# Performance work log

Measured on AMD Instinct MI355X. Metric: run time of the kernel, lower is better.

The kernel has to match this reference:

```python
import jax, jax.numpy as jnp
import numpy as np

HIDDEN = 1024
INTER = 2048
NUM_EXPERTS = 8
TOP_K = 2
GROUP_SIZE = 128
TOKENS = 4096


def _dequant_int4(packed, scale, group_size):
    # packed: [E, N, K//2] ints in [0,256) holding two uint4 nibbles (low | high<<4)
    # scale:  [E, N, K//group_size] float32
    E, N, Kh = packed.shape
    K = 2 * Kh
    low = packed & 0xF
    high = (packed >> 4) & 0xF
    # interleave: even K positions = low nibble, odd = high nibble
    q = jnp.stack([low, high], axis=-1).reshape(E, N, K) - 8  # int4 values in [-8,7]
    q = q.astype(jnp.float32).reshape(E, N, K // group_size, group_size)
    w = q * scale[..., None]
    return w.reshape(E, N, K)


def setup_inputs() -> dict:
    key = jax.random.key(0)
    k1, k2, k3, k4, k5, k6 = jax.random.split(key, 6)
    x = jax.random.normal(k1, (TOKENS, HIDDEN), dtype=jnp.float32)
    router_w = jax.random.normal(k2, (NUM_EXPERTS, HIDDEN), dtype=jnp.float32) * 0.02
    w1 = jax.random.randint(k3, (NUM_EXPERTS, 2 * INTER, HIDDEN // 2), 0, 256, dtype=jnp.int32)
    w1_scale = jax.random.uniform(k4, (NUM_EXPERTS, 2 * INTER, HIDDEN // GROUP_SIZE), dtype=jnp.float32) * 0.05
    w2 = jax.random.randint(k5, (NUM_EXPERTS, HIDDEN, INTER // 2), 0, 256, dtype=jnp.int32)
    w2_scale = jax.random.uniform(k6, (NUM_EXPERTS, HIDDEN, INTER // GROUP_SIZE), dtype=jnp.float32) * 0.05
    return {"x": x, "router_w": router_w, "w1": w1, "w1_scale": w1_scale, "w2": w2, "w2_scale": w2_scale}


def reference(x, router_w, w1, w1_scale, w2, w2_scale):
    # Router: topk then softmax over the top-k logits
    scores = x @ router_w.T                                 # [T, E]
    top_w, top_i = jax.lax.top_k(scores, TOP_K)             # [T, K]
    top_w = jax.nn.softmax(top_w, axis=-1).astype(jnp.float32)

    # Dequantize int4 grouped weights once
    w1_deq = _dequant_int4(w1, w1_scale, GROUP_SIZE)        # [E, 2I, H]
    w2_deq = _dequant_int4(w2, w2_scale, GROUP_SIZE)        # [E, H, I]

    out = jnp.zeros_like(x)
    for e in range(NUM_EXPERTS):
        # per-token routing weight for expert e (0 if not routed)
        ge = jnp.sum(top_w * (top_i == e), axis=-1)         # [T]
        h = x @ w1_deq[e].T                                  # [T, 2I]
        gate, up = h[:, :INTER], h[:, INTER:]
        a = jax.nn.silu(gate) * up                           # SwiGLU
        y = a @ w2_deq[e].T                                  # [T, H]
        out = out + ge[:, None] * y
    return out
```

## Files before the change

### kernel.cpp

```cpp
#include <hip/hip_runtime.h>
#include <hip/hip_bf16.h>

#define HIDDEN 1024
#define INTER 2048
#define NE 8
#define GS 128
#define TOKENS 4096
#define MAXROWS 9216
#define MAXTILES 72
#define MAXT256 40

typedef __bf16 bf16x8 __attribute__((ext_vector_type(8)));
typedef float f32x4 __attribute__((ext_vector_type(4)));

#define OFF_TOPKI 0u
#define OFF_TOPKW 32768u
#define OFF_CTRL  65536u
#define OFF_TOK   66048u
#define OFF_SLOT  102912u
#define OFF_TILE  135680u
#define OFF_T256  136192u
#define OFF_V256  136448u
#define OFF_XB    139776u
#define OFF_A     8530432u
#define OFF_W1D   46279168u
#define OFF_W2D   113388032u
#define OFF_Y0    OFF_W1D
#define OFF_Y1    (OFF_W1D + 18874368u)

__device__ __forceinline__ unsigned short f2bf(float f) {
  union { float f; unsigned int u; } v; v.f = f;
  unsigned int r = (v.u + 0x7FFFu + ((v.u >> 16) & 1u)) >> 16;
  return (unsigned short)r;
}
__device__ __forceinline__ float bf2f(unsigned int u) {
  union { unsigned int u; float f; } v; v.u = u << 16;
  return v.f;
}
__device__ __forceinline__ unsigned int pack2(unsigned short lo, unsigned short hi) {
  return (unsigned int)lo | ((unsigned int)hi << 16);
}

typedef const __attribute__((address_space(1))) unsigned int GAS;
typedef __attribute__((address_space(3))) unsigned int LAS;
__device__ __forceinline__ void gload16(const unsigned short* g, unsigned short* l) {
  __builtin_amdgcn_global_load_lds((GAS*)g, (LAS*)l, 16, 0, 0);
}

__global__ __launch_bounds__(256) void k_prep(const float* __restrict__ x,
    const float* __restrict__ rw, int* __restrict__ topki, float* __restrict__ topkw,
    const int* __restrict__ w1, const float* __restrict__ w1s,
    unsigned short* __restrict__ w1d,
    const int* __restrict__ w2, const float* __restrict__ w2s,
    unsigned short* __restrict__ w2d, unsigned short* __restrict__ xb) {
  int bid = blockIdx.x, tid = threadIdx.x;
  if (bid == 7168) {
    uint2 z; z.x = 0u; z.y = 0u;
    *reinterpret_cast<uint2*>(xb + (size_t)TOKENS * HIDDEN + tid * 4) = z;
    return;
  }
  if (bid >= 5120) {
    size_t base = (size_t)(bid - 5120) * 4096 + tid * 4;
    int4 p[4];
#pragma unroll
    for (int c = 0; c < 4; c++)
      p[c] = *reinterpret_cast<const int4*>(w2 + base + c * 1024);
#pragma unroll
    for (int c = 0; c < 4; c++) {
      size_t i4 = base + c * 1024;
      int r = (int)(i4 >> 10);
      int i = (int)(i4 & 1023);
      float s = w2s[r * 16 + (i >> 6)];
      int pv[4] = { p[c].x, p[c].y, p[c].z, p[c].w };
      uint4 o; unsigned int ov[4];
#pragma unroll
      for (int j = 0; j < 4; j++) {
        float lo = (float)((pv[j] & 15) - 8) * s;
        float hi = (float)(((pv[j] >> 4) & 15) - 8) * s;
        ov[j] = pack2(f2bf(lo), f2bf(hi));
      }
      o.x = ov[0]; o.y = ov[1]; o.z = ov[2]; o.w = ov[3];
      *reinterpret_cast<uint4*>(w2d + 2 * i4) = o;
    }
    return;
  }
  if (bid >= 1024) {
    size_t base = (size_t)(bid - 1024) * 4096 + tid * 4;
    int4 p[4];
#pragma unroll
    for (int c = 0; c < 4; c++)
      p[c] = *reinterpret_cast<const int4*>(w1 + base + c * 1024);
#pragma unroll
    for (int c = 0; c < 4; c++) {
      size_t i4 = base + c * 1024;
      int r = (int)(i4 >> 9);
      int i = (int)(i4 & 511);
      float s = w1s[r * 8 + (i >> 6)];
      int pv[4] = { p[c].x, p[c].y, p[c].z, p[c].w };
      uint4 o; unsigned int ov[4];
#pragma unroll
      for (int j = 0; j < 4; j++) {
        float lo = (float)((pv[j] & 15) - 8) * s;
        float hi = (float)(((pv[j] >> 4) & 15) - 8) * s;
        ov[j] = pack2(f2bf(lo), f2bf(hi));
      }
      o.x = ov[0]; o.y = ov[1]; o.z = ov[2]; o.w = ov[3];
      *reinterpret_cast<uint4*>(w1d + 2 * i4) = o;
    }
    return;
  }
  int wave = tid >> 6, lane = tid & 63;
  int t = bid * 4 + wave;
  const float* xr = x + (size_t)t * HIDDEN;
  float acc[NE];
#pragma unroll
  for (int e = 0; e < NE; e++) acc[e] = 0.f;
#pragma unroll
  for (int j = 0; j < 4; j++) {
    int col = j * 256 + lane * 4;
    float4 xv = *reinterpret_cast<const float4*>(xr + col);
    uint2 o;
    o.x = pack2(f2bf(xv.x), f2bf(xv.y));
    o.y = pack2(f2bf(xv.z), f2bf(xv.w));
    *reinterpret_cast<uint2*>(xb + (size_t)t * HIDDEN + col) = o;
#pragma unroll
    for (int e = 0; e < NE; e++) {
      float4 wv = *reinterpret_cast<const float4*>(rw + e * HIDDEN + col);
      acc[e] += xv.x * wv.x + xv.y * wv.y + xv.z * wv.z + xv.w * wv.w;
    }
  }
#pragma unroll
  for (int e = 0; e < NE; e++) {
    float v = acc[e];
    for (int off = 32; off > 0; off >>= 1) v += __shfl_down(v, off, 64);
    acc[e] = v;
  }
  if (lane == 0) {
    int b0 = 0; float s0 = acc[0];
#pragma unroll
    for (int e = 1; e < NE; e++) if (acc[e] > s0) { s0 = acc[e]; b0 = e; }
    int b1 = -1; float s1 = -3.0e38f;
#pragma unroll
    for (int e = 0; e < NE; e++) if (e != b0 && acc[e] > s1) { s1 = acc[e]; b1 = e; }
    float w0 = 1.f / (1.f + __expf(s1 - s0));
    topki[t * 2] = b0; topki[t * 2 + 1] = b1;
    topkw[t * 2] = w0; topkw[t * 2 + 1] = 1.f - w0;
  }
}

__global__ __launch_bounds__(256) void k_route2(const int* __restrict__ topki,
    int* __restrict__ ctrl, int* __restrict__ tok, int* __restrict__ slots,
    int* __restrict__ tilemap, int* __restrict__ tile256, int* __restrict__ valid256) {
  __shared__ int h[NE], off[NE], cnt[NE];
  int tid = threadIdx.x;
  if (tid < NE) h[tid] = 0;
  __syncthreads();
  for (int i = tid; i < TOKENS * 2; i += 256) atomicAdd(&h[topki[i]], 1);
  __syncthreads();
  if (tid == 0) {
    int run = 0, t = 0, t2 = 0;
    for (int e = 0; e < NE; e++) {
      int c = h[e];
      ctrl[e] = c; ctrl[16 + e] = run; off[e] = run;
      int pc = (c + 127) & ~127;
      int m = pc >> 7;
      for (int mt = 0; mt < m; mt++) tilemap[t++] = (e << 20) | (run + mt * 128);
      int n2 = (m + 1) >> 1;
      for (int i2 = 0; i2 < n2; i2++) {
        int st = i2 * 256;
        if (st + 256 > pc) st = (pc >= 256) ? (pc - 256) : 0;
        tile256[t2] = (e << 20) | (run + st);
        int v = pc - st; valid256[t2] = (v < 256) ? v : 256;
        t2++;
      }
      run += pc;
    }
    ctrl[24] = run; ctrl[25] = t; ctrl[26] = t2;
  }
  __syncthreads();
#pragma unroll
  for (int e = 0; e < NE; e++) {
    int c = h[e], pc = (c + 127) & ~127;
    for (int i = c + tid; i < pc; i += 256) tok[off[e] + i] = -1;
  }
  if (tid < NE) cnt[tid] = off[tid];
  __syncthreads();
  for (int i = tid; i < TOKENS * 2; i += 256) {
    int e = topki[i];
    int p = atomicAdd(&cnt[e], 1);
    tok[p] = i >> 1;
    slots[i] = p;
  }
}

__global__ __launch_bounds__(256) void k_gemm1(
    const unsigned short* __restrict__ xb, const unsigned short* __restrict__ w1d,
    const int* __restrict__ ctrl, const int* __restrict__ tilemap,
    const int* __restrict__ tok, unsigned short* __restrict__ a_out) {
  __shared__ unsigned short sA[128 * 32];
  __shared__ unsigned short sBg[64 * 32];
  __shared__ unsigned short sBu[64 * 32];
  int bid = blockIdx.x, tid = threadIdx.x;
  int nt = bid & 31, tile = bid >> 5;
  if (tile >= ctrl[25]) return;
  int tm = tilemap[tile];
  int e = tm >> 20, row0 = tm & 0xFFFFF;
  int n0 = nt * 64;
  int wave = tid >> 6, lane = tid & 63;
  int ln = lane & 15, quad = lane >> 4;
  int wr = (wave & 1) * 64, wc = (wave >> 1) * 32;

  int srow = tid >> 2, scblk = tid & 3;
  int scol = (scblk ^ ((srow >> 1) & 3)) * 8;
  int t0 = tok[row0 + srow];
  int t1 = tok[row0 + 64 + srow];
  const unsigned short* gA0 = xb + (size_t)(t0 < 0 ? TOKENS : t0) * HIDDEN + scol;
  const unsigned short* gA1 = xb + (size_t)(t1 < 0 ? TOKENS : t1) * HIDDEN + scol;
  const unsigned short* gBg = w1d + ((size_t)e * 4096 + n0 + srow) * HIDDEN + scol;
  const unsigned short* gBu = gBg + (size_t)INTER * HIDDEN;
  unsigned short* lA0 = sA + tid * 8;
  unsigned short* lA1 = sA + 64 * 32 + tid * 8;
  unsigned short* lBg = sBg + tid * 8;
  unsigned short* lBu = sBu + tid * 8;

  f32x4 aG[4][2] = {}, aU[4][2] = {};
  for (int k0 = 0; k0 < HIDDEN; k0 += 32) {
    __syncthreads();
    gload16(gA0 + k0, lA0);
    gload16(gA1 + k0, lA1);
    gload16(gBg + k0, lBg);
    gload16(gBu + k0, lBu);
    __syncthreads();
    bf16x8 af[4], bg[2], bu[2];
#pragma unroll
    for (int m = 0; m < 4; m++) {
      int ar = wr + m * 16 + ln;
      af[m] = *reinterpret_cast<const bf16x8*>(&sA[ar * 32 + (quad ^ ((ar >> 1) & 3)) * 8]);
    }
#pragma unroll
    for (int n = 0; n < 2; n++) {
      int br = wc + n * 16 + ln;
      int bo = br * 32 + (quad ^ ((br >> 1) & 3)) * 8;
      bg[n] = *reinterpret_cast<const bf16x8*>(&sBg[bo]);
      bu[n] = *reinterpret_cast<const bf16x8*>(&sBu[bo]);
    }
#pragma unroll
    for (int m = 0; m < 4; m++)
#pragma unroll
      for (int n = 0; n < 2; n++) {
        aG[m][n] = __builtin_amdgcn_mfma_f32_16x16x32_bf16(af[m], bg[n], aG[m][n], 0, 0, 0);
        aU[m][n] = __builtin_amdgcn_mfma_f32_16x16x32_bf16(af[m], bu[n], aU[m][n], 0, 0, 0);
      }
  }
#pragma unroll
  for (int m = 0; m < 4; m++)
#pragma unroll
    for (int n = 0; n < 2; n++) {
      int col = n0 + wc + n * 16 + ln;
#pragma unroll
      for (int r = 0; r < 4; r++) {
        float g = aG[m][n][r], u = aU[m][n][r];
        float act = (g / (1.f + __expf(-g))) * u;
        int row = row0 + wr + m * 16 + quad * 4 + r;
        a_out[(size_t)row * INTER + col] = f2bf(act);
      }
    }
}

__global__ __launch_bounds__(256) void k_gemm2(
    const unsigned short* __restrict__ a_in, const unsigned short* __restrict__ w2d,
    const int* __restrict__ ctrl, const int* __restrict__ tilemap,
    unsigned short* __restrict__ y) {
  __shared__ unsigned short sA[128 * 32];
  __shared__ unsigned short sB[128 * 32];
  int bid = blockIdx.x, tid = threadIdx.x;
  int kp = bid & 1, nt = (bid >> 1) & 7, tile = bid >> 4;
  if (tile >= ctrl[25]) return;
  int tm = tilemap[tile];
  int e = tm >> 20, row0 = tm & 0xFFFFF;
  int n0 = nt * 128;
  int wave = tid >> 6, lane = tid & 63;
  int ln = lane & 15, quad = lane >> 4;
  int wr = (wave & 1) * 64, wc = (wave >> 1) * 64;

  int srow = tid >> 2, scblk = tid & 3;
  int scol = (scblk ^ ((srow >> 1) & 3)) * 8;
  int kbase = kp * (INTER / 2);
  const unsigned short* gA0 = a_in + (size_t)(row0 + srow) * INTER + kbase + scol;
  const unsigned short* gA1 = gA0 + (size_t)64 * INTER;
  const unsigned short* gB0 = w2d + ((size_t)e * 1024 + n0 + srow) * INTER + kbase + scol;
  const unsigned short* gB1 = gB0 + (size_t)64 * INTER;
  unsigned short* lA0 = sA + tid * 8;
  unsigned short* lA1 = sA + 64 * 32 + tid * 8;
  unsigned short* lB0 = sB + tid * 8;
  unsigned short* lB1 = sB + 64 * 32 + tid * 8;

  f32x4 acc[4][4] = {};
  for (int k0 = 0; k0 < INTER / 2; k0 += 32) {
    __syncthreads();
    gload16(gA0 + k0, lA0);
    gload16(gA1 + k0, lA1);
    gload16(gB0 + k0, lB0);
    gload16(gB1 + k0, lB1);
    __syncthreads();
    bf16x8 af[4], bf_[4];
#pragma unroll
    for (int m = 0; m < 4; m++) {
      int ar = wr + m * 16 + ln;
      af[m] = *reinterpret_cast<const bf16x8*>(&sA[ar * 32 + (quad ^ ((ar >> 1) & 3)) * 8]);
    }
#pragma unroll
    for (int n = 0; n < 4; n++) {
      int br = wc + n * 16 + ln;
      bf_[n] = *reinterpret_cast<const bf16x8*>(&sB[br * 32 + (quad ^ ((br >> 1) & 3)) * 8]);
    }
#pragma unroll
    for (int m = 0; m < 4; m++)
#pragma unroll
      for (int n = 0; n < 4; n++)
        acc[m][n] = __builtin_amdgcn_mfma_f32_16x16x32_bf16(af[m], bf_[n], acc[m][n], 0, 0, 0);
  }
  unsigned short* yk = y + (size_t)kp * MAXROWS * HIDDEN;
#pragma unroll
  for (int m = 0; m < 4; m++)
#pragma unroll
    for (int n = 0; n < 4; n++) {
      int col = n0 + wc + n * 16 + ln;
#pragma unroll
      for (int r = 0; r < 4; r++) {
        int row = row0 + wr + m * 16 + quad * 4 + r;
        yk[(size_t)row * HIDDEN + col] = f2bf(acc[m][n][r]);
      }
    }
}

__global__ __launch_bounds__(256) void k_combine(const unsigned short* __restrict__ y,
    const int* __restrict__ slots, const float* __restrict__ topkw,
    float* __restrict__ out) {
  int t = blockIdx.x;
  int c = threadIdx.x * 4;
  int s0 = slots[t * 2], s1 = slots[t * 2 + 1];
  float g0 = topkw[t * 2], g1 = topkw[t * 2 + 1];
  const unsigned short* y1 = y + (size_t)MAXROWS * HIDDEN;
  uint2 a0 = *reinterpret_cast<const uint2*>(y  + (size_t)s0 * HIDDEN + c);
  uint2 a1 = *reinterpret_cast<const uint2*>(y1 + (size_t)s0 * HIDDEN + c);
  uint2 b0 = *reinterpret_cast<const uint2*>(y  + (size_t)s1 * HIDDEN + c);
  uint2 b1 = *reinterpret_cast<const uint2*>(y1 + (size_t)s1 * HIDDEN + c);
  float4 o;
  o.x = g0 * (bf2f(a0.x & 0xffffu) + bf2f(a1.x & 0xffffu))
      + g1 * (bf2f(b0.x & 0xffffu) + bf2f(b1.x & 0xffffu));
  o.y = g0 * (bf2f(a0.x >> 16) + bf2f(a1.x >> 16))
      + g1 * (bf2f(b0.x >> 16) + bf2f(b1.x >> 16));
  o.z = g0 * (bf2f(a0.y & 0xffffu) + bf2f(a1.y & 0xffffu))
      + g1 * (bf2f(b0.y & 0xffffu) + bf2f(b1.y & 0xffffu));
  o.w = g0 * (bf2f(a0.y >> 16) + bf2f(a1.y >> 16))
      + g1 * (bf2f(b0.y >> 16) + bf2f(b1.y >> 16));
  *reinterpret_cast<float4*>(out + (size_t)t * HIDDEN + c) = o;
}

extern "C" void kernel_launch(void* const* d_in, const int* in_sizes, int n_in,
                              void* d_out, int out_size, void* d_ws, size_t ws_size,
                              hipStream_t stream) {
  const float* x   = (const float*)d_in[0];
  const float* rw  = (const float*)d_in[1];
  const int*   w1  = (const int*)d_in[2];
  const float* w1s = (const float*)d_in[3];
  const int*   w2  = (const int*)d_in[4];
  const float* w2s = (const float*)d_in[5];
  float* out = (float*)d_out;
  char* ws = (char*)d_ws;

  int*   topki = (int*)(ws + OFF_TOPKI);
  float* topkw = (float*)(ws + OFF_TOPKW);
  int*   ctrl  = (int*)(ws + OFF_CTRL);
  int*   tok   = (int*)(ws + OFF_TOK);
  int*   slots = (int*)(ws + OFF_SLOT);
  int*   tilemap = (int*)(ws + OFF_TILE);
  int*   tile256 = (int*)(ws + OFF_T256);
  int*   valid256 = (int*)(ws + OFF_V256);
  unsigned short* xb  = (unsigned short*)(ws + OFF_XB);
  unsigned short* a   = (unsigned short*)(ws + OFF_A);
  unsigned short* w1d = (unsigned short*)(ws + OFF_W1D);
  unsigned short* w2d = (unsigned short*)(ws + OFF_W2D);
  unsigned short* y   = (unsigned short*)(ws + OFF_Y0);

  k_prep<<<7169, 256, 0, stream>>>(x, rw, topki, topkw, w1, w1s, w1d, w2, w2s, w2d, xb);
  k_route2<<<1, 256, 0, stream>>>(topki, ctrl, tok, slots, tilemap, tile256, valid256);
  k_gemm1<<<32 * MAXTILES, 256, 0, stream>>>(xb, w1d, ctrl, tilemap, tok, a);
  k_gemm2<<<16 * MAXTILES, 256, 0, stream>>>(a, w2d, ctrl, tilemap, y);
  k_combine<<<TOKENS, 256, 0, stream>>>(y, slots, topkw, out);
}
```

Before: 325.7 us.

## Fuse int4 weight dequantization into both expert GEMM B-tile loads

Drops the separate pass that expanded all int4 weights to bf16 in a workspace buffer. Each GEMM block now loads packed int32 words and dequantizes them in registers with a magic-number float trick and a packed bf16 convert, then writes the bf16 values to shared memory. This removes a large write and re-read of bf16 weights in exchange for repeated dequant work in every block that shares an expert's weights. The B loads also become synchronous register loads instead of direct-to-LDS loads, which may stall more per k-step.

```diff
diff --git a/kernel.cpp b/kernel.cpp
--- a/kernel.cpp
+++ b/kernel.cpp
@@ -23,10 +23,8 @@
 #define OFF_V256  136448u
 #define OFF_XB    139776u
 #define OFF_A     8530432u
-#define OFF_W1D   46279168u
-#define OFF_W2D   113388032u
-#define OFF_Y0    OFF_W1D
-#define OFF_Y1    (OFF_W1D + 18874368u)
+#define OFF_Y0    46279168u
+#define OFF_Y1    (OFF_Y0 + 18874368u)
 
 __device__ __forceinline__ unsigned short f2bf(float f) {
   union { float f; unsigned int u; } v; v.f = f;
@@ -47,66 +45,32 @@
   __builtin_amdgcn_global_load_lds((GAS*)g, (LAS*)l, 16, 0, 0);
 }
 
+__device__ __forceinline__ uint4 deq8(int4 p, float s, float c) {
+  unsigned int pv[4] = { (unsigned int)p.x, (unsigned int)p.y,
+                         (unsigned int)p.z, (unsigned int)p.w };
+  unsigned int ov[4];
+#pragma unroll
+  for (int j = 0; j < 4; j++) {
+    unsigned int v = pv[j];
+    float flo = __uint_as_float(0x43000000u | ((v & 15u) << 16));
+    float fhi = __uint_as_float(0x43000000u | ((v << 12) & 0x000F0000u));
+    float lo = __builtin_fmaf(flo, s, c);
+    float hi = __builtin_fmaf(fhi, s, c);
+    unsigned int pk;
+    asm("v_cvt_pk_bf16_f32 %0, %1, %2" : "=v"(pk) : "v"(lo), "v"(hi));
+    ov[j] = pk;
+  }
+  uint4 o; o.x = ov[0]; o.y = ov[1]; o.z = ov[2]; o.w = ov[3];
+  return o;
+}
+
 __global__ __launch_bounds__(256) void k_prep(const float* __restrict__ x,
     const float* __restrict__ rw, int* __restrict__ topki, float* __restrict__ topkw,
-    const int* __restrict__ w1, const float* __restrict__ w1s,
-    unsigned short* __restrict__ w1d,
-    const int* __restrict__ w2, const float* __restrict__ w2s,
-    unsigned short* __restrict__ w2d, unsigned short* __restrict__ xb) {
+    unsigned short* __restrict__ xb) {
   int bid = blockIdx.x, tid = threadIdx.x;
-  if (bid == 7168) {
+  if (bid == 1024) {
     uint2 z; z.x = 0u; z.y = 0u;
     *reinterpret_cast<uint2*>(xb + (size_t)TOKENS * HIDDEN + tid * 4) = z;
-    return;
-  }
-  if (bid >= 5120) {
-    size_t base = (size_t)(bid - 5120) * 4096 + tid * 4;
-    int4 p[4];
-#pragma unroll
-    for (int c = 0; c < 4; c++)
-      p[c] = *reinterpret_cast<const int4*>(w2 + base + c * 1024);
-#pragma unroll
-    for (int c = 0; c < 4; c++) {
-      size_t i4 = base + c * 1024;
-      int r = (int)(i4 >> 10);
-      int i = (int)(i4 & 1023);
-      float s = w2s[r * 16 + (i >> 6)];
-      int pv[4] = { p[c].x, p[c].y, p[c].z, p[c].w };
-      uint4 o; unsigned int ov[4];
-#pragma unroll
-      for (int j = 0; j < 4; j++) {
-        float lo = (float)((pv[j] & 15) - 8) * s;
-        float hi = (float)(((pv[j] >> 4) & 15) - 8) * s;
-        ov[j] = pack2(f2bf(lo), f2bf(hi));
-      }
-      o.x = ov[0]; o.y = ov[1]; o.z = ov[2]; o.w = ov[3];
-      *reinterpret_cast<uint4*>(w2d + 2 * i4) = o;
-    }
-    return;
-  }
-  if (bid >= 1024) {
-    size_t base = (size_t)(bid - 1024) * 4096 + tid * 4;
-    int4 p[4];
-#pragma unroll
-    for (int c = 0; c < 4; c++)
-      p[c] = *reinterpret_cast<const int4*>(w1 + base + c * 1024);
-#pragma unroll
-    for (int c = 0; c < 4; c++) {
-      size_t i4 = base + c * 1024;
-      int r = (int)(i4 >> 9);
-      int i = (int)(i4 & 511);
-      float s = w1s[r * 8 + (i >> 6)];
-      int pv[4] = { p[c].x, p[c].y, p[c].z, p[c].w };
-      uint4 o; unsigned int ov[4];
-#pragma unroll
-      for (int j = 0; j < 4; j++) {
-        float lo = (float)((pv[j] & 15) - 8) * s;
-        float hi = (float)(((pv[j] >> 4) & 15) - 8) * s;
-        ov[j] = pack2(f2bf(lo), f2bf(hi));
-      }
-      o.x = ov[0]; o.y = ov[1]; o.z = ov[2]; o.w = ov[3];
-      *reinterpret_cast<uint4*>(w1d + 2 * i4) = o;
-    }
     return;
   }
   int wave = tid >> 6, lane = tid & 63;
@@ -194,9 +158,10 @@
 }
 
 __global__ __launch_bounds__(256) void k_gemm1(
-    const unsigned short* __restrict__ xb, const unsigned short* __restrict__ w1d,
-    const int* __restrict__ ctrl, const int* __restrict__ tilemap,
-    const int* __restrict__ tok, unsigned short* __restrict__ a_out) {
+    const unsigned short* __restrict__ xb, const int* __restrict__ w1,
+    const float* __restrict__ w1s, const int* __restrict__ ctrl,
+    const int* __restrict__ tilemap, const int* __restrict__ tok,
+    unsigned short* __restrict__ a_out) {
   __shared__ unsigned short sA[128 * 32];
   __shared__ unsigned short sBg[64 * 32];
   __shared__ unsigned short sBu[64 * 32];
@@ -210,47 +175,58 @@
   int ln = lane & 15, quad = lane >> 4;
   int wr = (wave & 1) * 64, wc = (wave >> 1) * 32;
 
-  int srow = tid >> 2, scblk = tid & 3;
-  int scol = (scblk ^ ((srow >> 1) & 3)) * 8;
+  int srow = tid >> 2;
+  int gcb = (tid & 3) ^ ((srow >> 1) & 3);
+  int scol = gcb * 8;
   int t0 = tok[row0 + srow];
   int t1 = tok[row0 + 64 + srow];
   const unsigned short* gA0 = xb + (size_t)(t0 < 0 ? TOKENS : t0) * HIDDEN + scol;
   const unsigned short* gA1 = xb + (size_t)(t1 < 0 ? TOKENS : t1) * HIDDEN + scol;
-  const unsigned short* gBg = w1d + ((size_t)e * 4096 + n0 + srow) * HIDDEN + scol;
-  const unsigned short* gBu = gBg + (size_t)INTER * HIDDEN;
+  const int* gPg = w1 + (((size_t)e * 4096 + n0 + srow) << 9) + gcb * 4;
+  const int* gPu = gPg + ((size_t)2048 << 9);
+  const float* sWg = w1s + ((size_t)e * 4096 + n0 + srow) * 8;
+  const float* sWu = sWg + 2048 * 8;
   unsigned short* lA0 = sA + tid * 8;
   unsigned short* lA1 = sA + 64 * 32 + tid * 8;
   unsigned short* lBg = sBg + tid * 8;
   unsigned short* lBu = sBu + tid * 8;
 
   f32x4 aG[4][2] = {}, aU[4][2] = {};
-  for (int k0 = 0; k0 < HIDDEN; k0 += 32) {
-    __syncthreads();
-    gload16(gA0 + k0, lA0);
-    gload16(gA1 + k0, lA1);
-    gload16(gBg + k0, lBg);
-    gload16(gBu + k0, lBu);
-    __syncthreads();
-    bf16x8 af[4], bg[2], bu[2];
-#pragma unroll
-    for (int m = 0; m < 4; m++) {
-      int ar = wr + m * 16 + ln;
-      af[m] = *reinterpret_cast<const bf16x8*>(&sA[ar * 32 + (quad ^ ((ar >> 1) & 3)) * 8]);
-    }
-#pragma unroll
-    for (int n = 0; n < 2; n++) {
-      int br = wc + n * 16 + ln;
-      int bo = br * 32 + (quad ^ ((br >> 1) & 3)) * 8;
-      bg[n] = *reinterpret_cast<const bf16x8*>(&sBg[bo]);
-      bu[n] = *reinterpret_cast<const bf16x8*>(&sBu[bo]);
-    }
-#pragma unroll
-    for (int m = 0; m < 4; m++)
+  for (int g = 0; g < 8; g++) {
+    float sg_ = sWg[g], su_ = sWu[g];
+    float cg = -136.f * sg_, cu = -136.f * su_;
+#pragma unroll
+    for (int kk = 0; kk < 4; kk++) {
+      int k0 = g * 128 + kk * 32;
+      __syncthreads();
+      gload16(gA0 + k0, lA0);
+      gload16(gA1 + k0, lA1);
+      int4 pg = *reinterpret_cast<const int4*>(gPg + (k0 >> 1));
+      int4 pu = *reinterpret_cast<const int4*>(gPu + (k0 >> 1));
+      *reinterpret_cast<uint4*>(lBg) = deq8(pg, sg_, cg);
+      *reinterpret_cast<uint4*>(lBu) = deq8(pu, su_, cu);
+      __syncthreads();
+      bf16x8 af[4], bg[2], bu[2];
+#pragma unroll
+      for (int m = 0; m < 4; m++) {
+        int ar = wr + m * 16 + ln;
+        af[m] = *reinterpret_cast<const bf16x8*>(&sA[ar * 32 + (quad ^ ((ar >> 1) & 3)) * 8]);
+      }
 #pragma unroll
       for (int n = 0; n < 2; n++) {
-        aG[m][n] = __builtin_amdgcn_mfma_f32_16x16x32_bf16(af[m], bg[n], aG[m][n], 0, 0, 0);
-        aU[m][n] = __builtin_amdgcn_mfma_f32_16x16x32_bf16(af[m], bu[n], aU[m][n], 0, 0, 0);
-      }
+        int br = wc + n * 16 + ln;
+        int bo = br * 32 + (quad ^ ((br >> 1) & 3)) * 8;
+        bg[n] = *reinterpret_cast<const bf16x8*>(&sBg[bo]);
+        bu[n] = *reinterpret_cast<const bf16x8*>(&sBu[bo]);
+      }
+#pragma unroll
+      for (int m = 0; m < 4; m++)
+#pragma unroll
+        for (int n = 0; n < 2; n++) {
+          aG[m][n] = __builtin_amdgcn_mfma_f32_16x16x32_bf16(af[m], bg[n], aG[m][n], 0, 0, 0);
+          aU[m][n] = __builtin_amdgcn_mfma_f32_16x16x32_bf16(af[m], bu[n], aU[m][n], 0, 0, 0);
+        }
+    }
   }
 #pragma unroll
   for (int m = 0; m < 4; m++)
@@ -268,9 +244,9 @@
 }
 
 __global__ __launch_bounds__(256) void k_gemm2(
-    const unsigned short* __restrict__ a_in, const unsigned short* __restrict__ w2d,
-    const int* __restrict__ ctrl, const int* __restrict__ tilemap,
-    unsigned short* __restrict__ y) {
+    const unsigned short* __restrict__ a_in, const int* __restrict__ w2,
+    const float* __restrict__ w2s, const int* __restrict__ ctrl,
+    const int* __restrict__ tilemap, unsigned short* __restrict__ y) {
   __shared__ unsigned short sA[128 * 32];
   __shared__ unsigned short sB[128 * 32];
   int bid = blockIdx.x, tid = threadIdx.x;
@@ -283,42 +259,53 @@
   int ln = lane & 15, quad = lane >> 4;
   int wr = (wave & 1) * 64, wc = (wave >> 1) * 64;
 
-  int srow = tid >> 2, scblk = tid & 3;
-  int scol = (scblk ^ ((srow >> 1) & 3)) * 8;
+  int srow = tid >> 2;
+  int gcb = (tid & 3) ^ ((srow >> 1) & 3);
+  int scol = gcb * 8;
   int kbase = kp * (INTER / 2);
   const unsigned short* gA0 = a_in + (size_t)(row0 + srow) * INTER + kbase + scol;
   const unsigned short* gA1 = gA0 + (size_t)64 * INTER;
-  const unsigned short* gB0 = w2d + ((size_t)e * 1024 + n0 + srow) * INTER + kbase + scol;
-  const unsigned short* gB1 = gB0 + (size_t)64 * INTER;
+  const int* gP0 = w2 + ((size_t)e * 1024 + n0 + srow) * 1024 + (kbase >> 1) + gcb * 4;
+  const int* gP1 = gP0 + (size_t)64 * 1024;
+  const float* sW0 = w2s + ((size_t)e * 1024 + n0 + srow) * 16 + kp * 8;
+  const float* sW1 = sW0 + 64 * 16;
   unsigned short* lA0 = sA + tid * 8;
   unsigned short* lA1 = sA + 64 * 32 + tid * 8;
   unsigned short* lB0 = sB + tid * 8;
   unsigned short* lB1 = sB + 64 * 32 + tid * 8;
 
   f32x4 acc[4][4] = {};
-  for (int k0 = 0; k0 < INTER / 2; k0 += 32) {
-    __syncthreads();
-    gload16(gA0 + k0, lA0);
-    gload16(gA1 + k0, lA1);
-    gload16(gB0 + k0, lB0);
-    gload16(gB1 + k0, lB1);
-    __syncthreads();
-    bf16x8 af[4], bf_[4];
-#pragma unroll
-    for (int m = 0; m < 4; m++) {
-      int ar = wr + m * 16 + ln;
-      af[m] = *reinterpret_cast<const bf16x8*>(&sA[ar * 32 + (quad ^ ((ar >> 1) & 3)) * 8]);
-    }
-#pragma unroll
-    for (int n = 0; n < 4; n++) {
-      int br = wc + n * 16 + ln;
-      bf_[n] = *reinterpret_cast<const bf16x8*>(&sB[br * 32 + (quad ^ ((br >> 1) & 3)) * 8]);
-    }
-#pragma unroll
-    for (int m = 0; m < 4; m++)
-#pragma unroll
-      for (int n = 0; n < 4; n++)
-        acc[m][n] = __builtin_amdgcn_mfma_f32_16x16x32_bf16(af[m], bf_[n], acc[m][n], 0, 0, 0);
+  for (int g = 0; g < 8; g++) {
+    float s0_ = sW0[g], s1_ = sW1[g];
+    float c0 = -136.f * s0_, c1 = -136.f * s1_;
+#pragma unroll
+    for (int kk = 0; kk < 4; kk++) {
+      int k0 = g * 128 + kk * 32;
+      __syncthreads();
+      gload16(gA0 + k0, lA0);
+      gload16(gA1 + k0, lA1);
+      int4 p0 = *reinterpret_cast<const int4*>(gP0 + (k0 >> 1));
+      int4 p1 = *reinterpret_cast<const int4*>(gP1 + (k0 >> 1));
+      *reinterpret_cast<uint4*>(lB0) = deq8(p0, s0_, c0);
+      *reinterpret_cast<uint4*>(lB1) = deq8(p1, s1_, c1);
+      __syncthreads();
+      bf16x8 af[4], bf_[4];
+#pragma unroll
+      for (int m = 0; m < 4; m++) {
+        int ar = wr + m * 16 + ln;
+        af[m] = *reinterpret_cast<const bf16x8*>(&sA[ar * 32 + (quad ^ ((ar >> 1) & 3)) * 8]);
+      }
+#pragma unroll
+      for (int n = 0; n < 4; n++) {
+        int br = wc + n * 16 + ln;
+        bf_[n] = *reinterpret_cast<const bf16x8*>(&sB[br * 32 + (quad ^ ((br >> 1) & 3)) * 8]);
+      }
+#pragma unroll
+      for (int m = 0; m < 4; m++)
+#pragma unroll
+        for (int n = 0; n < 4; n++)
+          acc[m][n] = __builtin_amdgcn_mfma_f32_16x16x32_bf16(af[m], bf_[n], acc[m][n], 0, 0, 0);
+    }
   }
   unsigned short* yk = y + (size_t)kp * MAXROWS * HIDDEN;
 #pragma unroll
@@ -380,13 +367,11 @@
   int*   valid256 = (int*)(ws + OFF_V256);
   unsigned short* xb  = (unsigned short*)(ws + OFF_XB);
   unsigned short* a   = (unsigned short*)(ws + OFF_A);
-  unsigned short* w1d = (unsigned short*)(ws + OFF_W1D);
-  unsigned short* w2d = (unsigned short*)(ws + OFF_W2D);
   unsigned short* y   = (unsigned short*)(ws + OFF_Y0);
 
-  k_prep<<<7169, 256, 0, stream>>>(x, rw, topki, topkw, w1, w1s, w1d, w2, w2s, w2d, xb);
+  k_prep<<<1025, 256, 0, stream>>>(x, rw, topki, topkw, xb);
   k_route2<<<1, 256, 0, stream>>>(topki, ctrl, tok, slots, tilemap, tile256, valid256);
-  k_gemm1<<<32 * MAXTILES, 256, 0, stream>>>(xb, w1d, ctrl, tilemap, tok, a);
-  k_gemm2<<<16 * MAXTILES, 256, 0, stream>>>(a, w2d, ctrl, tilemap, y);
+  k_gemm1<<<32 * MAXTILES, 256, 0, stream>>>(xb, w1, w1s, ctrl, tilemap, tok, a);
+  k_gemm2<<<16 * MAXTILES, 256, 0, stream>>>(a, w2, w2s, ctrl, tilemap, y);
   k_combine<<<TOKENS, 256, 0, stream>>>(y, slots, topkw, out);
 }
```

Measured after the change: 399.5 us. +22.7%, slower.
